# Optimization experiments

Measured on AMD Instinct MI355X. Metric: run time of the kernel, lower is better.

Reference implementation:

```python
import jax, jax.numpy as jnp
import numpy as np

N_NODES = 100000
N_EDGES = 1600000
VOCAB = 10000
HIDDEN = 64
LAYERS = 3
N_GRAPHS = 512
OUT_DIM = 1


def setup_inputs() -> dict:
    key = jax.random.key(0)
    ks = jax.random.split(key, 8)
    feats = jax.random.randint(ks[0], (N_NODES,), 0, VOCAB)
    src = jax.random.randint(ks[1], (N_EDGES,), 0, N_NODES)
    dst = jax.random.randint(ks[2], (N_EDGES,), 0, N_NODES)
    graph_ids = jnp.sort(jax.random.randint(ks[3], (N_NODES,), 0, N_GRAPHS))
    emb_table = jax.random.normal(ks[4], (VOCAB, HIDDEN), jnp.float32) * 0.02
    Ws = jax.random.normal(ks[5], (LAYERS, HIDDEN, HIDDEN), jnp.float32) * (HIDDEN ** -0.5)
    bs = jnp.zeros((LAYERS, HIDDEN), jnp.float32)
    W_reg = jax.random.normal(ks[6], (HIDDEN, OUT_DIM), jnp.float32) * (HIDDEN ** -0.5)
    return {"feats": feats, "src": src, "dst": dst, "graph_ids": graph_ids,
            "n_graphs": N_GRAPHS, "emb_table": emb_table, "Ws": Ws, "bs": bs,
            "W_reg": W_reg}


def reference(feats, src, dst, graph_ids, n_graphs, emb_table, Ws, bs, W_reg):
    N = feats.shape[0]
    ones = jnp.ones(src.shape[0], jnp.float32)
    # DGL GraphConv norm='both': src normalized by out-degree^-1/2, dst by in-degree^-1/2,
    # degrees clamped to min 1 (allow_zero_in_degree=True).
    out_deg = jnp.maximum(jax.ops.segment_sum(ones, src, num_segments=N), 1.0)
    in_deg = jnp.maximum(jax.ops.segment_sum(ones, dst, num_segments=N), 1.0)
    norm_src = (out_deg ** -0.5)[:, None]  # [N,1]
    norm_dst = (in_deg ** -0.5)[:, None]
    h = emb_table[feats]  # [N, hidden]
    for i in range(Ws.shape[0]):  # fixed small layer count
        m = h * norm_src
        agg = jax.ops.segment_sum(m[src], dst, num_segments=N)  # SpMM scatter-add
        h = agg * norm_dst @ Ws[i] + bs[i]
        # dropout p=0 -> identity
    pooled = jax.ops.segment_sum(h, graph_ids, num_segments=n_graphs)  # SumPooling
    return pooled @ W_reg
```

## Files before the change

kernel.cpp:

```cpp
#include <hip/hip_runtime.h>

#define HIDDEN 64
#define RANGE 512
#define RSHIFT 9
#define RB 256
#define NWR 512
#define CAPC 56
#define RCAP 12288

__global__ __launch_bounds__(256) void pre_kernel(const float* __restrict__ emb,
                                                  const float* __restrict__ Ws,
                                                  const float* __restrict__ bs,
                                                  const float* __restrict__ Wreg,
                                                  float* __restrict__ wt,
                                                  float* __restrict__ embu, int V,
                                                  const int* __restrict__ src,
                                                  const int* __restrict__ dst,
                                                  unsigned* __restrict__ pairs,
                                                  unsigned short* __restrict__ srcb,
                                                  int* __restrict__ cnts_in,
                                                  int* __restrict__ cnts_out,
                                                  float* __restrict__ out, int out_n,
                                                  int E, int EC, int R) {
    __shared__ float u3[HIDDEN], u2[HIDDEN], u1[HIDDEN];
    __shared__ int cin[RB], cout[RB];
    int t = threadIdx.x;
    int b = blockIdx.x;
    const float* W0 = Ws;
    const float* W1 = Ws + HIDDEN * HIDDEN;
    const float* W2 = Ws + 2 * HIDDEN * HIDDEN;
    if (t < HIDDEN) { float s = 0.f; for (int j = 0; j < HIDDEN; j++) s += W2[t*HIDDEN+j] * Wreg[j]; u3[t] = s; }
    __syncthreads();
    if (t < HIDDEN) { float s = 0.f; for (int j = 0; j < HIDDEN; j++) s += W1[t*HIDDEN+j] * u3[j]; u2[t] = s; }
    __syncthreads();
    if (t < HIDDEN) { float s = 0.f; for (int j = 0; j < HIDDEN; j++) s += W0[t*HIDDEN+j] * u2[j]; u1[t] = s; }
    __syncthreads();
    if (b == 0) {
        if (t < HIDDEN) {
            float c1v = bs[t] * u2[t];
            float c2v = bs[HIDDEN + t] * u3[t];
            float c3v = bs[2*HIDDEN + t] * Wreg[t];
#pragma unroll
            for (int off = 32; off > 0; off >>= 1) {
                c1v += __shfl_down(c1v, off, 64);
                c2v += __shfl_down(c2v, off, 64);
                c3v += __shfl_down(c3v, off, 64);
            }
            if (t == 0) { wt[64] = c1v; wt[65] = c2v; wt[66] = c3v; }
        }
        for (int i = t; i < out_n; i += 256) out[i] = 0.0f;
    }
    int lane = t & 63, warp = t >> 6, vs = lane >> 4, ln = lane & 15;
    int EV = (V + 15) >> 4;
    for (int task = b; task < EV; task += gridDim.x) {
        int v = task * 16 + warp * 4 + vs;
        if (v < V) {
            const float* row = emb + (size_t)v * HIDDEN;
            float acc = row[ln]*u1[ln] + row[16+ln]*u1[16+ln]
                      + row[32+ln]*u1[32+ln] + row[48+ln]*u1[48+ln];
            acc += __shfl_xor(acc, 1, 64);
            acc += __shfl_xor(acc, 2, 64);
            acc += __shfl_xor(acc, 4, 64);
            acc += __shfl_xor(acc, 8, 64);
            if (ln == 0) embu[v] = acc;
        }
    }
    for (int i = t; i < RB; i += 256) { cin[i] = 0; cout[i] = 0; }
    __syncthreads();
    int es = b * EC, ee = min(E, es + EC);
    for (int e = es + t; e < ee; e += 256) {
        int s = src[e], d = dst[e];
        int r = d >> RSHIFT;
        int lr = atomicAdd(&cin[r], 1);
        if (lr < CAPC)
            pairs[((size_t)r * NWR + b) * CAPC + lr] =
                ((unsigned)(d - (r << RSHIFT)) << 17) | (unsigned)s;
        int r2 = s >> RSHIFT;
        int lr2 = atomicAdd(&cout[r2], 1);
        if (lr2 < CAPC)
            srcb[((size_t)r2 * NWR + b) * CAPC + lr2] = (unsigned short)(s - (r2 << RSHIFT));
    }
    __syncthreads();
    for (int i = t; i < R; i += 256) {
        cnts_in[(size_t)i * NWR + b]  = min(cin[i], CAPC);
        cnts_out[(size_t)i * NWR + b] = min(cout[i], CAPC);
    }
}

__global__ __launch_bounds__(256) void build_kernel(const unsigned* __restrict__ pairs,
                                                    const unsigned short* __restrict__ srcb,
                                                    const int* __restrict__ cnts_in,
                                                    const int* __restrict__ cnts_out,
                                                    const int* __restrict__ feats,
                                                    const float* __restrict__ embu,
                                                    int* __restrict__ rbeg,
                                                    int* __restrict__ rend,
                                                    int* __restrict__ col,
                                                    float* __restrict__ ndst,
                                                    float* __restrict__ nsrc,
                                                    float* __restrict__ y0,
                                                    int N) {
    __shared__ int cnt[RANGE];
    __shared__ int sc[RANGE];
    __shared__ int oh[RANGE];
    __shared__ int tmp[256];
    __shared__ int ccin[NWR], ccout[NWR];
    int r = blockIdx.x, t = threadIdx.x;
    int n0 = r << RSHIFT;
    int nn = min(RANGE, N - n0);
    for (int i = t; i < RANGE; i += 256) { cnt[i] = 0; oh[i] = 0; }
    for (int i = t; i < NWR; i += 256) {
        ccin[i]  = cnts_in[(size_t)r * NWR + i];
        ccout[i] = cnts_out[(size_t)r * NWR + i];
    }
    __syncthreads();
    for (int b = t; b < NWR; b += 256) {
        const uint4* cell = (const uint4*)(pairs + ((size_t)r * NWR + b) * CAPC);
        int c = ccin[b];
        for (int k = 0; k < c; k += 4) {
            uint4 q = cell[k >> 2];
            atomicAdd(&cnt[q.x >> 17], 1);
            if (k + 1 < c) atomicAdd(&cnt[q.y >> 17], 1);
            if (k + 2 < c) atomicAdd(&cnt[q.z >> 17], 1);
            if (k + 3 < c) atomicAdd(&cnt[q.w >> 17], 1);
        }
    }
    for (int b = t; b < NWR; b += 256) {
        const unsigned* cell = (const unsigned*)(srcb + ((size_t)r * NWR + b) * CAPC);
        int c = ccout[b];
        for (int k = 0; k < c; k += 2) {
            unsigned q = cell[k >> 1];
            atomicAdd(&oh[q & 0xffff], 1);
            if (k + 1 < c) atomicAdd(&oh[q >> 16], 1);
        }
    }
    __syncthreads();
    int a0 = cnt[2 * t], a1 = cnt[2 * t + 1];
    tmp[t] = a0 + a1;
    __syncthreads();
    for (int off = 1; off < 256; off <<= 1) {
        int u = (t >= off) ? tmp[t - off] : 0;
        __syncthreads();
        tmp[t] += u;
        __syncthreads();
    }
    int c_in = tmp[255];
    int pre = (t > 0) ? tmp[t - 1] : 0;
    sc[2 * t] = pre;
    sc[2 * t + 1] = pre + a0;
    __syncthreads();
    int base = r * RCAP;
    for (int i = t; i < nn; i += 256) {
        int n = n0 + i;
        rbeg[n] = base + sc[i];
        rend[n] = base + sc[i] + cnt[i];
        ndst[n] = rsqrtf(fmaxf((float)cnt[i], 1.0f));
        float ns = rsqrtf(fmaxf((float)oh[i], 1.0f));
        nsrc[n] = ns;
        y0[n] = embu[feats[n]] * ns;
    }
    if (t < 32) col[base + c_in + t] = 0;
    __syncthreads();
    for (int b = t; b < NWR; b += 256) {
        const unsigned* cell = pairs + ((size_t)r * NWR + b) * CAPC;
        int c = ccin[b];
        for (int k = 0; k < c; k++) {
            unsigned w = cell[k];
            int slot = atomicAdd(&sc[w >> 17], 1);
            col[base + slot] = (int)(w & 0x1ffff);
        }
    }
}

__global__ __launch_bounds__(256) void sspmm_kernel(const int* __restrict__ rbeg,
                                                    const int* __restrict__ rend,
                                                    const int* __restrict__ col,
                                                    const float* __restrict__ y,
                                                    const float* __restrict__ ndst,
                                                    const float* __restrict__ nsrc,
                                                    const float* __restrict__ wt, int cidx,
                                                    float* __restrict__ out,
                                                    int N, int NH, int scale_out) {
    int lane = threadIdx.x & 63;
    int warp = threadIdx.x >> 6;
    int ns_ = lane >> 4, ln = lane & 15;
    int nA = blockIdx.x * 16 + warp * 4 + ns_;
    int nB = nA + NH;
    int begA = 0, endA = 0, begB = 0, endB = 0;
    if (nA < NH) { begA = rbeg[nA]; endA = rend[nA]; }
    if (nB < N)  { begB = rbeg[nB]; endB = rend[nB]; }
    float accA = 0.0f, accB = 0.0f;
    int jA = begA + ln, jB = begB + ln;
#pragma unroll
    for (int it = 0; it < 2; it++) {
        int ja = jA + (it << 4), jb = jB + (it << 4);
        float va = y[col[ja]];
        float vb = y[col[jb]];
        accA += (ja < endA) ? va : 0.0f;
        accB += (jb < endB) ? vb : 0.0f;
    }
    for (int j = jA + 32; j < endA; j += 16) accA += y[col[j]];
    for (int j = jB + 32; j < endB; j += 16) accB += y[col[j]];
#pragma unroll
    for (int m = 1; m <= 8; m <<= 1) {
        accA += __shfl_xor(accA, m, 64);
        accB += __shfl_xor(accB, m, 64);
    }
    if (ln == 0) {
        float c = wt[cidx];
        if (nA < NH) {
            float o = accA * ndst[nA] + c;
            out[nA] = scale_out ? o * nsrc[nA] : o;
        }
        if (nB < N) {
            float o = accB * ndst[nB] + c;
            out[nB] = scale_out ? o * nsrc[nB] : o;
        }
    }
}

__global__ __launch_bounds__(256) void final_kernel(const int* __restrict__ gids,
                                                    const float* __restrict__ nodeval,
                                                    float* __restrict__ out, int N) {
    int n = blockIdx.x * 256 + threadIdx.x;
    int lane = threadIdx.x & 63;
    float v = 0.0f;
    int g = -1;
    if (n < N) { v = nodeval[n]; g = gids[n]; }
#pragma unroll
    for (int off = 1; off < 64; off <<= 1) {
        float u = __shfl_up(v, off, 64);
        int gu = __shfl_up(g, off, 64);
        if (lane >= off && gu == g) v += u;
    }
    int gn = __shfl_down(g, 1, 64);
    bool last = (lane == 63) || (gn != g);
    if (n < N && last) atomicAdd(&out[g], v);
}

extern "C" void kernel_launch(void* const* d_in, const int* in_sizes, int n_in,
                              void* d_out, int out_size, void* d_ws, size_t ws_size,
                              hipStream_t stream) {
    const int*   feats = (const int*)d_in[0];
    const int*   src   = (const int*)d_in[1];
    const int*   dst   = (const int*)d_in[2];
    const int*   gids  = (const int*)d_in[3];
    const float* emb   = (const float*)d_in[5];
    const float* Ws    = (const float*)d_in[6];
    const float* bs    = (const float*)d_in[7];
    const float* Wreg  = (const float*)d_in[8];
    float* out = (float*)d_out;

    int N = in_sizes[0];
    int E = in_sizes[1];
    int V = in_sizes[5] / HIDDEN;
    int NB = (N + 255) / 256;
    int R = (N + RANGE - 1) / RANGE;
    int EC = (E + NWR - 1) / NWR;
    int NH = (N + 1) / 2;
    int GS = (NH + 15) / 16;

    char* p = (char*)d_ws;
    int*   rbeg    = (int*)p;    p += (size_t)N * 4;
    int*   rend    = (int*)p;    p += (size_t)N * 4;
    float* nsrc    = (float*)p;  p += (size_t)N * 4;
    float* ndst    = (float*)p;  p += (size_t)N * 4;
    float* wt      = (float*)p;  p += 128 * 4;
    float* embu    = (float*)p;  p += (size_t)V * 4;
    float* y0      = (float*)p;  p += (size_t)N * 4;
    float* y1      = (float*)p;  p += (size_t)N * 4;
    float* y2      = (float*)p;  p += (size_t)N * 4;
    float* nodeval = (float*)p;  p += (size_t)N * 4;
    int*   cnts_in  = (int*)p;   p += (size_t)R * NWR * 4;
    int*   cnts_out = (int*)p;   p += (size_t)R * NWR * 4;
    int*   col     = (int*)p;    p += (size_t)R * RCAP * 4;
    p = (char*)(((uintptr_t)p + 255) & ~(uintptr_t)255);
    unsigned* pairs = (unsigned*)p;            p += (size_t)R * NWR * CAPC * 4;
    unsigned short* srcb = (unsigned short*)p; p += (size_t)R * NWR * CAPC * 2;

    pre_kernel<<<NWR, 256, 0, stream>>>(emb, Ws, bs, Wreg, wt, embu, V,
                                        src, dst, pairs, srcb, cnts_in, cnts_out,
                                        out, out_size, E, EC, R);
    build_kernel<<<R, 256, 0, stream>>>(pairs, srcb, cnts_in, cnts_out, feats, embu,
                                        rbeg, rend, col, ndst, nsrc, y0, N);

    sspmm_kernel<<<GS, 256, 0, stream>>>(rbeg, rend, col, y0, ndst, nsrc, wt, 64, y1, N, NH, 1);
    sspmm_kernel<<<GS, 256, 0, stream>>>(rbeg, rend, col, y1, ndst, nsrc, wt, 65, y2, N, NH, 1);
    sspmm_kernel<<<GS, 256, 0, stream>>>(rbeg, rend, col, y2, ndst, nsrc, wt, 66, nodeval, N, NH, 0);
    final_kernel<<<NB, 256, 0, stream>>>(gids, nodeval, out, N);
}
```

Before: 170.7 us.

## Replace fixed-capacity edge bins with LDS counting-sort into compact per-block runs

The edge binning in pre_kernel now counts edges per destination/source range, prefix-sums them, scatters the packed edges into shared memory, and writes one contiguous compact run per block with per-range offsets. This drops the fixed CAPC-slot cells, which were sparse, padded and silently truncated on overflow. build_kernel reads the variable-length runs through the offsets. It costs an extra pass over src/dst and two block scans, and the build reads lose their uint4 vectorization and alignment.

```diff
diff --git a/kernel.cpp b/kernel.cpp
--- a/kernel.cpp
+++ b/kernel.cpp
@@ -5,7 +5,7 @@
 #define RSHIFT 9
 #define RB 256
 #define NWR 512
-#define CAPC 56
+#define ECMAX 3328
 #define RCAP 12288
 
 __global__ __launch_bounds__(256) void pre_kernel(const float* __restrict__ emb,
@@ -19,11 +19,16 @@
                                                   unsigned* __restrict__ pairs,
                                                   unsigned short* __restrict__ srcb,
                                                   int* __restrict__ cnts_in,
+                                                  int* __restrict__ offs_in,
                                                   int* __restrict__ cnts_out,
+                                                  int* __restrict__ offs_out,
                                                   float* __restrict__ out, int out_n,
                                                   int E, int EC, int R) {
     __shared__ float u3[HIDDEN], u2[HIDDEN], u1[HIDDEN];
-    __shared__ int cin[RB], cout[RB];
+    __shared__ int hin[RB], hout[RB];
+    __shared__ int tmp[256];
+    __shared__ unsigned plds[ECMAX];
+    __shared__ unsigned short slds[ECMAX];
     int t = threadIdx.x;
     int b = blockIdx.x;
     const float* W0 = Ws;
@@ -65,32 +70,65 @@
             if (ln == 0) embu[v] = acc;
         }
     }
-    for (int i = t; i < RB; i += 256) { cin[i] = 0; cout[i] = 0; }
+    for (int i = t; i < RB; i += 256) { hin[i] = 0; hout[i] = 0; }
     __syncthreads();
     int es = b * EC, ee = min(E, es + EC);
+    int cntE = ee - es;
+    for (int e = es + t; e < ee; e += 256) {
+        atomicAdd(&hin[dst[e] >> RSHIFT], 1);
+        atomicAdd(&hout[src[e] >> RSHIFT], 1);
+    }
+    __syncthreads();
+    int vin = hin[t], vout = hout[t];
+    tmp[t] = vin;
+    __syncthreads();
+    for (int off = 1; off < 256; off <<= 1) {
+        int u = (t >= off) ? tmp[t - off] : 0;
+        __syncthreads();
+        tmp[t] += u;
+        __syncthreads();
+    }
+    int ein = tmp[t] - vin;
+    tmp[t] = vout;
+    __syncthreads();
+    for (int off = 1; off < 256; off <<= 1) {
+        int u = (t >= off) ? tmp[t - off] : 0;
+        __syncthreads();
+        tmp[t] += u;
+        __syncthreads();
+    }
+    int eout = tmp[t] - vout;
+    if (t < R) {
+        cnts_in [(size_t)t * NWR + b] = vin;
+        offs_in [(size_t)t * NWR + b] = ein;
+        cnts_out[(size_t)t * NWR + b] = vout;
+        offs_out[(size_t)t * NWR + b] = eout;
+    }
+    hin[t] = ein;
+    hout[t] = eout;
+    __syncthreads();
     for (int e = es + t; e < ee; e += 256) {
         int s = src[e], d = dst[e];
         int r = d >> RSHIFT;
-        int lr = atomicAdd(&cin[r], 1);
-        if (lr < CAPC)
-            pairs[((size_t)r * NWR + b) * CAPC + lr] =
-                ((unsigned)(d - (r << RSHIFT)) << 17) | (unsigned)s;
+        int lr = atomicAdd(&hin[r], 1);
+        plds[lr] = ((unsigned)(d - (r << RSHIFT)) << 17) | (unsigned)s;
         int r2 = s >> RSHIFT;
-        int lr2 = atomicAdd(&cout[r2], 1);
-        if (lr2 < CAPC)
-            srcb[((size_t)r2 * NWR + b) * CAPC + lr2] = (unsigned short)(s - (r2 << RSHIFT));
-    }
-    __syncthreads();
-    for (int i = t; i < R; i += 256) {
-        cnts_in[(size_t)i * NWR + b]  = min(cin[i], CAPC);
-        cnts_out[(size_t)i * NWR + b] = min(cout[i], CAPC);
-    }
+        int lr2 = atomicAdd(&hout[r2], 1);
+        slds[lr2] = (unsigned short)(s - (r2 << RSHIFT));
+    }
+    __syncthreads();
+    unsigned* pg = pairs + (size_t)b * EC;
+    unsigned short* sg = srcb + (size_t)b * EC;
+    for (int i = t; i < cntE; i += 256) pg[i] = plds[i];
+    for (int i = t; i < cntE; i += 256) sg[i] = slds[i];
 }
 
 __global__ __launch_bounds__(256) void build_kernel(const unsigned* __restrict__ pairs,
                                                     const unsigned short* __restrict__ srcb,
                                                     const int* __restrict__ cnts_in,
+                                                    const int* __restrict__ offs_in,
                                                     const int* __restrict__ cnts_out,
+                                                    const int* __restrict__ offs_out,
                                                     const int* __restrict__ feats,
                                                     const float* __restrict__ embu,
                                                     int* __restrict__ rbeg,
@@ -99,40 +137,32 @@
                                                     float* __restrict__ ndst,
                                                     float* __restrict__ nsrc,
                                                     float* __restrict__ y0,
-                                                    int N) {
+                                                    int N, int EC) {
     __shared__ int cnt[RANGE];
     __shared__ int sc[RANGE];
     __shared__ int oh[RANGE];
     __shared__ int tmp[256];
-    __shared__ int ccin[NWR], ccout[NWR];
+    __shared__ int ccin[NWR], coin[NWR], ccout[NWR], coout[NWR];
     int r = blockIdx.x, t = threadIdx.x;
     int n0 = r << RSHIFT;
     int nn = min(RANGE, N - n0);
     for (int i = t; i < RANGE; i += 256) { cnt[i] = 0; oh[i] = 0; }
     for (int i = t; i < NWR; i += 256) {
-        ccin[i]  = cnts_in[(size_t)r * NWR + i];
+        ccin[i]  = cnts_in [(size_t)r * NWR + i];
+        coin[i]  = offs_in [(size_t)r * NWR + i];
         ccout[i] = cnts_out[(size_t)r * NWR + i];
+        coout[i] = offs_out[(size_t)r * NWR + i];
     }
     __syncthreads();
     for (int b = t; b < NWR; b += 256) {
-        const uint4* cell = (const uint4*)(pairs + ((size_t)r * NWR + b) * CAPC);
+        const unsigned* run = pairs + (size_t)b * EC + coin[b];
         int c = ccin[b];
-        for (int k = 0; k < c; k += 4) {
-            uint4 q = cell[k >> 2];
-            atomicAdd(&cnt[q.x >> 17], 1);
-            if (k + 1 < c) atomicAdd(&cnt[q.y >> 17], 1);
-            if (k + 2 < c) atomicAdd(&cnt[q.z >> 17], 1);
-            if (k + 3 < c) atomicAdd(&cnt[q.w >> 17], 1);
-        }
+        for (int k = 0; k < c; k++) atomicAdd(&cnt[run[k] >> 17], 1);
     }
     for (int b = t; b < NWR; b += 256) {
-        const unsigned* cell = (const unsigned*)(srcb + ((size_t)r * NWR + b) * CAPC);
+        const unsigned short* run = srcb + (size_t)b * EC + coout[b];
         int c = ccout[b];
-        for (int k = 0; k < c; k += 2) {
-            unsigned q = cell[k >> 1];
-            atomicAdd(&oh[q & 0xffff], 1);
-            if (k + 1 < c) atomicAdd(&oh[q >> 16], 1);
-        }
+        for (int k = 0; k < c; k++) atomicAdd(&oh[run[k]], 1);
     }
     __syncthreads();
     int a0 = cnt[2 * t], a1 = cnt[2 * t + 1];
@@ -162,10 +192,10 @@
     if (t < 32) col[base + c_in + t] = 0;
     __syncthreads();
     for (int b = t; b < NWR; b += 256) {
-        const unsigned* cell = pairs + ((size_t)r * NWR + b) * CAPC;
+        const unsigned* run = pairs + (size_t)b * EC + coin[b];
         int c = ccin[b];
         for (int k = 0; k < c; k++) {
-            unsigned w = cell[k];
+            unsigned w = run[k];
             int slot = atomicAdd(&sc[w >> 17], 1);
             col[base + slot] = (int)(w & 0x1ffff);
         }
@@ -272,17 +302,20 @@
     float* y2      = (float*)p;  p += (size_t)N * 4;
     float* nodeval = (float*)p;  p += (size_t)N * 4;
     int*   cnts_in  = (int*)p;   p += (size_t)R * NWR * 4;
+    int*   offs_in  = (int*)p;   p += (size_t)R * NWR * 4;
     int*   cnts_out = (int*)p;   p += (size_t)R * NWR * 4;
+    int*   offs_out = (int*)p;   p += (size_t)R * NWR * 4;
     int*   col     = (int*)p;    p += (size_t)R * RCAP * 4;
     p = (char*)(((uintptr_t)p + 255) & ~(uintptr_t)255);
-    unsigned* pairs = (unsigned*)p;            p += (size_t)R * NWR * CAPC * 4;
-    unsigned short* srcb = (unsigned short*)p; p += (size_t)R * NWR * CAPC * 2;
+    unsigned* pairs = (unsigned*)p;            p += (size_t)NWR * EC * 4;
+    unsigned short* srcb = (unsigned short*)p; p += (size_t)NWR * EC * 2;
 
     pre_kernel<<<NWR, 256, 0, stream>>>(emb, Ws, bs, Wreg, wt, embu, V,
-                                        src, dst, pairs, srcb, cnts_in, cnts_out,
+                                        src, dst, pairs, srcb,
+                                        cnts_in, offs_in, cnts_out, offs_out,
                                         out, out_size, E, EC, R);
-    build_kernel<<<R, 256, 0, stream>>>(pairs, srcb, cnts_in, cnts_out, feats, embu,
-                                        rbeg, rend, col, ndst, nsrc, y0, N);
+    build_kernel<<<R, 256, 0, stream>>>(pairs, srcb, cnts_in, offs_in, cnts_out, offs_out,
+                                        feats, embu, rbeg, rend, col, ndst, nsrc, y0, N, EC);
 
     sspmm_kernel<<<GS, 256, 0, stream>>>(rbeg, rend, col, y0, ndst, nsrc, wt, 64, y1, N, NH, 1);
     sspmm_kernel<<<GS, 256, 0, stream>>>(rbeg, rend, col, y1, ndst, nsrc, wt, 65, y2, N, NH, 1);
```

Result: faster. 165.9 us (-2.8%).
